# Optimization experiments

Measured on AMD Instinct MI355X. Metric: run time of the kernel, lower is better.

## Reference

```python
import jax, jax.numpy as jnp
import numpy as np

T_STEPS, N = 8192, 2048
SPIKE_THRESHOLD = 30.0


def setup_inputs() -> dict:
    key = jax.random.key(0)
    k_x, k_w = jax.random.split(key, 2)
    w_mean, w_var = 0.15, 0.25
    x_in = jax.random.normal(k_x, (T_STEPS, N), dtype=jnp.float32)
    # rand_ws = w_mean - w_var + 2*w_var*rand(N,N)
    w = w_mean - w_var + 2.0 * w_var * jax.random.uniform(k_w, (N, N), dtype=jnp.float32)
    v_rest = jnp.full((N,), -65.0, dtype=jnp.float32)
    tau_m = jnp.full((N,), 4.0, dtype=jnp.float32)
    tau_g = jnp.full((N,), 2.0, dtype=jnp.float32)
    pre_c = jnp.float32(4.0)
    post_c = jnp.float32(130.0)
    v0 = jnp.zeros((N,), dtype=jnp.float32)
    g0 = jnp.zeros((N,), dtype=jnp.float32)
    return {"x_in": x_in, "w": w, "v_rest": v_rest, "tau_m": tau_m,
            "tau_g": tau_g, "pre_c": pre_c, "post_c": post_c, "v0": v0, "g0": g0}


def reference(x_in, w, v_rest, tau_m, tau_g, pre_c, post_c, v0, g0):
    # Faithful LIF_complex.forward, iterated over T timesteps via lax.scan.
    def step(carry, x_t):
        v, g = carry
        # synaptic input current
        I = post_c * jax.nn.sigmoid(pre_c * (w @ g + x_t))
        # conductance decay
        g = g - g / tau_g
        # membrane potential update
        v = v + (v_rest - v + I) / tau_m
        # soft spike surrogate (returned), hard spike for reset
        spiked_soft = jax.nn.sigmoid(v - SPIKE_THRESHOLD)
        spk = (v >= SPIKE_THRESHOLD).astype(v.dtype)
        not_spk = 1.0 - spk
        v = spk * v_rest + not_spk * v
        g = spk + not_spk * g
        return (v, g), (v, spiked_soft)

    _, (vs, spikeds) = jax.lax.scan(step, (v0, g0), x_in)
    # [2, T, N]: vs and soft-spike traces over time
    return jnp.stack([vs, spikeds])
```

## Files before the change

### kernel.cpp

```cpp
#include <hip/hip_runtime.h>
#include <cmath>


#define T_STEPS 8192
#define NN      2048
#define NBLK    128
#define NTHR    1024
#define RPB     16
#define DUMP    64
#define NSLOT   128
#define PADU    16

typedef unsigned long long u64;

__device__ __forceinline__ float stable_sigmoid(float x) {
    float E   = expf(-fabsf(x));
    float den = 1.0f + E;
    float num = (x >= 0.0f) ? 1.0f : E;
    return num / den;
}

#define DPP_ADD(acc, ctrl, rmask)                                         \
    acc += __int_as_float(__builtin_amdgcn_update_dpp(                    \
        0, __float_as_int(acc), ctrl, rmask, 0xF, true));

#define WAVE_RED(acc)            \
    DPP_ADD(acc, 0x111, 0xF)     \
    DPP_ADD(acc, 0x112, 0xF)     \
    DPP_ADD(acc, 0x114, 0xF)     \
    DPP_ADD(acc, 0x118, 0xF)     \
    DPP_ADD(acc, 0x142, 0xA)     \
    DPP_ADD(acc, 0x143, 0xC)

__global__ __launch_bounds__(NTHR, 2) void lif_kernel(
    const float* __restrict__ x_in,
    const float* __restrict__ w,
    const float* __restrict__ v_rest,
    const float* __restrict__ tau_m,
    const float* __restrict__ tau_g,
    const float* __restrict__ pre_cp,
    const float* __restrict__ post_cp,
    const float* __restrict__ v0,
    const float* __restrict__ g0,
    float* __restrict__ out,
    u64* __restrict__ slots)
{
    __shared__ unsigned sbits[NSLOT];
    __shared__ float preduce[2][4][RPB];
    __shared__ float vbuf[2][DUMP][RPB];
    __shared__ float sbuf[2][DUMP][RPB];

    const int tid = threadIdx.x;
    const int b   = blockIdx.x;
    const int wv  = tid >> 6;
    const int i   = wv & 3;
    const int j   = wv >> 2;
    const int k   = tid & 63;

    const float* wbase = w + (size_t)(b * RPB + 4 * i) * NN + 512 * j;
    const float4* r0 = (const float4*)(wbase);
    const float4* r1 = (const float4*)(wbase + NN);
    const float4* r2 = (const float4*)(wbase + 2 * NN);
    const float4* r3 = (const float4*)(wbase + 3 * NN);
    const float4 w0a = r0[2 * k], w0b = r0[2 * k + 1];
    const float4 w1a = r1[2 * k], w1b = r1[2 * k + 1];
    const float4 w2a = r2[2 * k], w2b = r2[2 * k + 1];
    const float4 w3a = r3[2 * k], w3b = r3[2 * k + 1];

    const int c0 = 512 * j + 8 * k;
    float4 ga = ((const float4*)(g0 + c0))[0];
    float4 gb = ((const float4*)(g0 + c0))[1];
    const float4 tga = ((const float4*)(tau_g + c0))[0];
    const float4 tgb = ((const float4*)(tau_g + c0))[1];
    const float4 rga = make_float4(1.0f / tga.x, 1.0f / tga.y,
                                   1.0f / tga.z, 1.0f / tga.w);
    const float4 rgb = make_float4(1.0f / tgb.x, 1.0f / tgb.y,
                                   1.0f / tgb.z, 1.0f / tgb.w);
    const int slot_i  = c0 >> 4;
    const int bitbase = c0 & 15;

    const float pre_c  = pre_cp[0];
    const float post_c = post_cp[0];

    float vr = 0.f, rtm = 0.f, v = 0.f;
    if (tid < RPB) {
        const int n = b * RPB + tid;
        vr  = v_rest[n];
        rtm = 1.0f / tau_m[n];
        v   = v0[n];
    }

    for (int t = 0; t < T_STEPS; ++t) {
        float x = 0.0f;
        if (tid < RPB) x = x_in[(size_t)t * NN + b * RPB + tid];

        float4 da = ga, db = gb;
        if (t != 0) {
            da.x = fmaf(-rga.x, ga.x, ga.x); da.y = fmaf(-rga.y, ga.y, ga.y);
            da.z = fmaf(-rga.z, ga.z, ga.z); da.w = fmaf(-rga.w, ga.w, ga.w);
            db.x = fmaf(-rgb.x, gb.x, gb.x); db.y = fmaf(-rgb.y, gb.y, gb.y);
            db.z = fmaf(-rgb.z, gb.z, gb.z); db.w = fmaf(-rgb.w, gb.w, gb.w);

            if (wv < 4) {
                const int s = ((wv & 1) << 6) | k;
                const u64* sl = slots +
                    ((size_t)((t - 1) & 1) * NSLOT + s) * PADU;
                const unsigned want = (unsigned)(t - 1);
                if (wv >= 2) __builtin_amdgcn_s_sleep(6);
                u64 A = __hip_atomic_load(sl, __ATOMIC_RELAXED,
                                          __HIP_MEMORY_SCOPE_AGENT);
                while ((unsigned)(A >> 32) != want) {
                    __builtin_amdgcn_s_sleep(1);
                    A = __hip_atomic_load(sl, __ATOMIC_RELAXED,
                                          __HIP_MEMORY_SCOPE_AGENT);
                }
                __hip_atomic_store(&sbits[s], (unsigned)A,
                                   __ATOMIC_RELAXED,
                                   __HIP_MEMORY_SCOPE_WORKGROUP);
            }
        }
        __syncthreads();

        if (t != 0) {
            const unsigned bits = sbits[slot_i] >> bitbase;
            ga.x = (bits &   1u) ? 1.0f : da.x;
            ga.y = (bits &   2u) ? 1.0f : da.y;
            ga.z = (bits &   4u) ? 1.0f : da.z;
            ga.w = (bits &   8u) ? 1.0f : da.w;
            gb.x = (bits &  16u) ? 1.0f : db.x;
            gb.y = (bits &  32u) ? 1.0f : db.y;
            gb.z = (bits &  64u) ? 1.0f : db.z;
            gb.w = (bits & 128u) ? 1.0f : db.w;
        }

        float a0 = 0.f, a1 = 0.f, a2 = 0.f, a3 = 0.f;
#define ROWFMA(acc, wa, wb)                                       \
        acc = fmaf(wa.x, ga.x, acc); acc = fmaf(wa.y, ga.y, acc); \
        acc = fmaf(wa.z, ga.z, acc); acc = fmaf(wa.w, ga.w, acc); \
        acc = fmaf(wb.x, gb.x, acc); acc = fmaf(wb.y, gb.y, acc); \
        acc = fmaf(wb.z, gb.z, acc); acc = fmaf(wb.w, gb.w, acc);
        ROWFMA(a0, w0a, w0b)
        ROWFMA(a1, w1a, w1b)
        ROWFMA(a2, w2a, w2b)
        ROWFMA(a3, w3a, w3b)
#undef ROWFMA
        WAVE_RED(a0)
        WAVE_RED(a1)
        WAVE_RED(a2)
        WAVE_RED(a3)
        if (k == 63)
            ((float4*)preduce[t & 1])[j * 4 + i] = make_float4(a0, a1, a2, a3);
        __syncthreads();

        if (tid < RPB) {
            const float* pr = (const float*)preduce[t & 1];
            float u = (pr[tid] + pr[tid + 16]) + (pr[tid + 32] + pr[tid + 48]);
            float I = post_c * stable_sigmoid(pre_c * (u + x));
            v = v + (vr - v + I) * rtm;
            bool spk = (v >= 30.0f);
            u64 bal = __ballot(spk);
            if (tid == 0) {
                u64 pk = ((u64)(unsigned)t << 32) | (bal & 0xFFFFull);
                __hip_atomic_store(slots + ((size_t)(t & 1) * NSLOT + b) * PADU,
                                   pk, __ATOMIC_RELAXED,
                                   __HIP_MEMORY_SCOPE_AGENT);
            }
            __builtin_amdgcn_sched_barrier(0);
            float soft = stable_sigmoid(v - 30.0f);
            v = spk ? vr : v;
            vbuf[(t >> 6) & 1][t & (DUMP - 1)][tid] = v;
            sbuf[(t >> 6) & 1][t & (DUMP - 1)][tid] = soft;
        }

        if ((t & (DUMP - 1)) == 0 && t != 0) {
            const int bb = ((t >> 6) & 1) ^ 1;
            const int t0 = t - DUMP;
            const int s  = tid >> 4;
            const int rr = tid & 15;
            size_t o = (size_t)(t0 + s) * NN + b * RPB + rr;
            out[o] = vbuf[bb][s][rr];
            out[(size_t)T_STEPS * NN + o] = sbuf[bb][s][rr];
        }
    }

    __syncthreads();
    {
        const int bb = ((T_STEPS - DUMP) >> 6) & 1;
        const int t0 = T_STEPS - DUMP;
        const int s  = tid >> 4;
        const int rr = tid & 15;
        size_t o = (size_t)(t0 + s) * NN + b * RPB + rr;
        out[o] = vbuf[bb][s][rr];
        out[(size_t)T_STEPS * NN + o] = sbuf[bb][s][rr];
    }
}

extern "C" void kernel_launch(void* const* d_in, const int* in_sizes, int n_in,
                              void* d_out, int out_size, void* d_ws, size_t ws_size,
                              hipStream_t stream) {
    const float* x_in   = (const float*)d_in[0];
    const float* w      = (const float*)d_in[1];
    const float* v_rest = (const float*)d_in[2];
    const float* tau_m  = (const float*)d_in[3];
    const float* tau_g  = (const float*)d_in[4];
    const float* pre_c  = (const float*)d_in[5];
    const float* post_c = (const float*)d_in[6];
    const float* v0     = (const float*)d_in[7];
    const float* g0     = (const float*)d_in[8];
    float* out = (float*)d_out;

    u64* slots = (u64*)d_ws;

    hipMemsetAsync(slots, 0xFF, 2 * NSLOT * PADU * sizeof(u64), stream);

    void* args[] = {
        (void*)&x_in, (void*)&w, (void*)&v_rest, (void*)&tau_m, (void*)&tau_g,
        (void*)&pre_c, (void*)&post_c, (void*)&v0, (void*)&g0,
        (void*)&out, (void*)&slots
    };
    hipLaunchCooperativeKernel((void*)lif_kernel, dim3(NBLK), dim3(NTHR),
                               args, 0, stream);
}
```

Measured before the change: 15.10 ms.

## Split rows across 256 blocks with 8 rows each to halve per-block work

Measured after the change: 19.68 ms. +30.3%, slower.

```diff
diff --git a/kernel.cpp b/kernel.cpp
--- a/kernel.cpp
+++ b/kernel.cpp
@@ -4,11 +4,11 @@
 
 #define T_STEPS 8192
 #define NN      2048
-#define NBLK    128
+#define NBLK    256
 #define NTHR    1024
-#define RPB     16
+#define RPB     8
 #define DUMP    64
-#define NSLOT   128
+#define NSLOT   256
 #define PADU    16
 
 typedef unsigned long long u64;
@@ -53,19 +53,15 @@
     const int tid = threadIdx.x;
     const int b   = blockIdx.x;
     const int wv  = tid >> 6;
-    const int i   = wv & 3;
-    const int j   = wv >> 2;
+    const int rlo = wv >> 2;
+    const int j   = wv & 3;
     const int k   = tid & 63;
 
-    const float* wbase = w + (size_t)(b * RPB + 4 * i) * NN + 512 * j;
-    const float4* r0 = (const float4*)(wbase);
-    const float4* r1 = (const float4*)(wbase + NN);
-    const float4* r2 = (const float4*)(wbase + 2 * NN);
-    const float4* r3 = (const float4*)(wbase + 3 * NN);
-    const float4 w0a = r0[2 * k], w0b = r0[2 * k + 1];
-    const float4 w1a = r1[2 * k], w1b = r1[2 * k + 1];
-    const float4 w2a = r2[2 * k], w2b = r2[2 * k + 1];
-    const float4 w3a = r3[2 * k], w3b = r3[2 * k + 1];
+    const float* wbase = w + (size_t)(b * RPB + rlo) * NN + 512 * j;
+    const float4* rl = (const float4*)(wbase);
+    const float4* rh = (const float4*)(wbase + 4 * NN);
+    const float4 wla = rl[2 * k], wlb = rl[2 * k + 1];
+    const float4 wha = rh[2 * k], whb = rh[2 * k + 1];
 
     const int c0 = 512 * j + 8 * k;
     float4 ga = ((const float4*)(g0 + c0))[0];
@@ -76,8 +72,7 @@
                                    1.0f / tga.z, 1.0f / tga.w);
     const float4 rgb = make_float4(1.0f / tgb.x, 1.0f / tgb.y,
                                    1.0f / tgb.z, 1.0f / tgb.w);
-    const int slot_i  = c0 >> 4;
-    const int bitbase = c0 & 15;
+    const int slot_i = c0 >> 3;
 
     const float pre_c  = pre_cp[0];
     const float post_c = post_cp[0];
@@ -102,11 +97,10 @@
             db.z = fmaf(-rgb.z, gb.z, gb.z); db.w = fmaf(-rgb.w, gb.w, gb.w);
 
             if (wv < 4) {
-                const int s = ((wv & 1) << 6) | k;
+                const int s = (wv << 6) | k;
                 const u64* sl = slots +
                     ((size_t)((t - 1) & 1) * NSLOT + s) * PADU;
                 const unsigned want = (unsigned)(t - 1);
-                if (wv >= 2) __builtin_amdgcn_s_sleep(6);
                 u64 A = __hip_atomic_load(sl, __ATOMIC_RELAXED,
                                           __HIP_MEMORY_SCOPE_AGENT);
                 while ((unsigned)(A >> 32) != want) {
@@ -114,15 +108,13 @@
                     A = __hip_atomic_load(sl, __ATOMIC_RELAXED,
                                           __HIP_MEMORY_SCOPE_AGENT);
                 }
-                __hip_atomic_store(&sbits[s], (unsigned)A,
-                                   __ATOMIC_RELAXED,
-                                   __HIP_MEMORY_SCOPE_WORKGROUP);
+                sbits[s] = (unsigned)A;
             }
         }
         __syncthreads();
 
         if (t != 0) {
-            const unsigned bits = sbits[slot_i] >> bitbase;
+            const unsigned bits = sbits[slot_i];
             ga.x = (bits &   1u) ? 1.0f : da.x;
             ga.y = (bits &   2u) ? 1.0f : da.y;
             ga.z = (bits &   4u) ? 1.0f : da.z;
@@ -133,34 +125,33 @@
             gb.w = (bits & 128u) ? 1.0f : db.w;
         }
 
-        float a0 = 0.f, a1 = 0.f, a2 = 0.f, a3 = 0.f;
+        float a0 = 0.f, a1 = 0.f;
 #define ROWFMA(acc, wa, wb)                                       \
         acc = fmaf(wa.x, ga.x, acc); acc = fmaf(wa.y, ga.y, acc); \
         acc = fmaf(wa.z, ga.z, acc); acc = fmaf(wa.w, ga.w, acc); \
         acc = fmaf(wb.x, gb.x, acc); acc = fmaf(wb.y, gb.y, acc); \
         acc = fmaf(wb.z, gb.z, acc); acc = fmaf(wb.w, gb.w, acc);
-        ROWFMA(a0, w0a, w0b)
-        ROWFMA(a1, w1a, w1b)
-        ROWFMA(a2, w2a, w2b)
-        ROWFMA(a3, w3a, w3b)
+        ROWFMA(a0, wla, wlb)
+        ROWFMA(a1, wha, whb)
 #undef ROWFMA
         WAVE_RED(a0)
         WAVE_RED(a1)
-        WAVE_RED(a2)
-        WAVE_RED(a3)
-        if (k == 63)
-            ((float4*)preduce[t & 1])[j * 4 + i] = make_float4(a0, a1, a2, a3);
+        if (k == 63) {
+            preduce[t & 1][j][rlo]     = a0;
+            preduce[t & 1][j][rlo + 4] = a1;
+        }
         __syncthreads();
 
         if (tid < RPB) {
             const float* pr = (const float*)preduce[t & 1];
-            float u = (pr[tid] + pr[tid + 16]) + (pr[tid + 32] + pr[tid + 48]);
+            float u = (pr[tid] + pr[tid + RPB]) +
+                      (pr[tid + 2 * RPB] + pr[tid + 3 * RPB]);
             float I = post_c * stable_sigmoid(pre_c * (u + x));
             v = v + (vr - v + I) * rtm;
             bool spk = (v >= 30.0f);
             u64 bal = __ballot(spk);
             if (tid == 0) {
-                u64 pk = ((u64)(unsigned)t << 32) | (bal & 0xFFFFull);
+                u64 pk = ((u64)(unsigned)t << 32) | (bal & 0xFFull);
                 __hip_atomic_store(slots + ((size_t)(t & 1) * NSLOT + b) * PADU,
                                    pk, __ATOMIC_RELAXED,
                                    __HIP_MEMORY_SCOPE_AGENT);
@@ -172,11 +163,11 @@
             sbuf[(t >> 6) & 1][t & (DUMP - 1)][tid] = soft;
         }
 
-        if ((t & (DUMP - 1)) == 0 && t != 0) {
+        if ((t & (DUMP - 1)) == 0 && t != 0 && tid < DUMP * RPB) {
             const int bb = ((t >> 6) & 1) ^ 1;
             const int t0 = t - DUMP;
-            const int s  = tid >> 4;
-            const int rr = tid & 15;
+            const int s  = tid >> 3;
+            const int rr = tid & 7;
             size_t o = (size_t)(t0 + s) * NN + b * RPB + rr;
             out[o] = vbuf[bb][s][rr];
             out[(size_t)T_STEPS * NN + o] = sbuf[bb][s][rr];
@@ -184,11 +175,11 @@
     }
 
     __syncthreads();
-    {
+    if (tid < DUMP * RPB) {
         const int bb = ((T_STEPS - DUMP) >> 6) & 1;
         const int t0 = T_STEPS - DUMP;
-        const int s  = tid >> 4;
-        const int rr = tid & 15;
+        const int s  = tid >> 3;
+        const int rr = tid & 7;
         size_t o = (size_t)(t0 + s) * NN + b * RPB + rr;
         out[o] = vbuf[bb][s][rr];
         out[(size_t)T_STEPS * NN + o] = sbuf[bb][s][rr];
```
